# Performance work log

Hardware: AMD Instinct MI355X
Metric: run time of the kernel (lower is better)

The kernel has to match this reference:

```python
import jax, jax.numpy as jnp
import numpy as np

B, M, N_DIM = 2048, 1024, 64


def setup_inputs() -> dict:
    key = jax.random.key(0)
    ks = jax.random.split(key, 6)
    X = jax.random.normal(ks[0], (B, N_DIM), dtype=jnp.float32)
    Mu0 = jax.random.normal(ks[1], (M, N_DIM), dtype=jnp.float32)
    Mu1 = jax.random.normal(ks[2], (M, N_DIM), dtype=jnp.float32)
    # diagonal variances must be positive
    S0 = jax.random.uniform(ks[3], (M, N_DIM), dtype=jnp.float32, minval=0.1, maxval=1.0)
    S1 = jax.random.uniform(ks[4], (M, N_DIM), dtype=jnp.float32, minval=0.1, maxval=1.0)
    Lam = jax.random.uniform(ks[5], (M,), dtype=jnp.float32, minval=0.01, maxval=1.0)
    Lam = Lam / jnp.sum(Lam)  # transport-plan weights sum to 1
    return {"X": X, "Mu0": Mu0, "Mu1": Mu1, "S0": S0, "S1": S1,
            "Lam": Lam, "t": 0.3, "epsilon": 0.5}


def reference(X, Mu0, Mu1, S0, S1, Lam, t, epsilon):
    # GMMflow_fast.calc_u with sparse coupling of M nonzero (i,j) pairs.
    eps2 = epsilon ** 2
    Ds = jnp.sqrt(4.0 * S0 * S1 + epsilon ** 4)            # [M, n]
    Cs = 0.5 * (Ds - eps2)                                  # [M, n]
    v = Mu1 - Mu0                                           # [M, n]
    Mut = (1.0 - t) * Mu0 + t * Mu1                         # [M, n]
    Sigma = ((1.0 - t) ** 2) * S0 + (t ** 2) * S1 + 2.0 * t * (1.0 - t) * (Cs + 0.5 * eps2)
    Pt = t * S1 + (1.0 - t) * Cs
    Qt = (1.0 - t) * S0 + t * Cs
    St = Pt - Qt - eps2 * t
    K = St / Sigma                                          # [M, n]

    Xd = X[:, None, :] - Mut[None, :, :]                    # [B, M, n]
    U = K[None, :, :] * Xd + v[None, :, :]                  # [B, M, n]

    # Gaussian log-prob plus (n/2) log(2*pi), matching the torch code:
    # log N(x; mu, Sigma) + n/2 log(2pi) = -0.5 * sum(d^2/Sigma + log Sigma)
    logw = -0.5 * jnp.sum(Xd * Xd / Sigma[None, :, :] + jnp.log(Sigma)[None, :, :], axis=-1)  # [B, M]
    logw = jnp.clip(logw, -50.0, 50.0)
    W = jnp.exp(logw) * Lam[None, :]                        # [B, M]

    u = jnp.einsum('bm,bmd->bd', W, U)                      # [B, n]
    norm = jnp.sum(W, axis=1, keepdims=True)                # [B, 1]
    return u / norm
```

## Files before the change

### kernel.cpp

```cpp
#include <hip/hip_runtime.h>
#include <math.h>


#define B_N 2048
#define M_N 1024
#define NSPLIT 16
#define BT 64
#define MS 64

typedef short bf16x8 __attribute__((ext_vector_type(8)));
typedef float f32x4 __attribute__((ext_vector_type(4)));

static __device__ __forceinline__ unsigned short bf16rn(float f) {
    union { float f; unsigned u; } v; v.f = f;
    unsigned r = v.u + 0x7FFF + ((v.u >> 16) & 1);
    return (unsigned short)(r >> 16);
}
static __device__ __forceinline__ float bf2f(unsigned short h) {
    union { unsigned u; float f; } v; v.u = ((unsigned)h) << 16;
    return v.f;
}
static __device__ __forceinline__ void st4(unsigned short* p, unsigned short a,
                                           unsigned short b, unsigned short c, unsigned short d) {
    union { unsigned short u[4]; float2 f; } t;
    t.u[0] = a; t.u[1] = b; t.u[2] = c; t.u[3] = d;
    *(float2*)p = t.f;
}

__global__ __launch_bounds__(256)
void prep_kernel(const float* __restrict__ Mu0, const float* __restrict__ Mu1,
                 const float* __restrict__ S0, const float* __restrict__ S1,
                 const float* __restrict__ T, const float* __restrict__ E,
                 unsigned short* __restrict__ B1h, unsigned short* __restrict__ B1l,
                 unsigned short* __restrict__ VTh, float* __restrict__ qArr) {
    __shared__ float sK[4 * 65];
    __shared__ float sG[4 * 65];
    const int tid = threadIdx.x;
    const int m0 = blockIdx.x * 4;
    const int mi = tid >> 6, d = tid & 63;
    const int m = m0 + mi;
    const float t = T[0], e = E[0];
    const float eps2 = e * e, eps4 = eps2 * eps2, omt = 1.f - t;
    int idx = m * 64 + d;
    float s0 = S0[idx], s1 = S1[idx];
    float mu0 = Mu0[idx], mu1 = Mu1[idx];
    float Ds = sqrtf(4.f * s0 * s1 + eps4);
    float Cs = 0.5f * (Ds - eps2);
    float sig = omt * omt * s0 + t * t * s1 + 2.f * t * omt * (Cs + 0.5f * eps2);
    float St = (t * s1 + omt * Cs) - (omt * s0 + t * Cs) - eps2 * t;
    float a = 1.f / sig;
    float K = St * a;
    float mut = omt * mu0 + t * mu1;
    float pp = -2.f * mut * a;
    float g = (mu1 - mu0) - K * mut;
    unsigned short ah = bf16rn(a);
    B1h[m * 128 + d] = ah;
    B1l[m * 128 + d] = bf16rn(a - bf2f(ah));
    unsigned short ph = bf16rn(pp);
    B1h[m * 128 + 64 + d] = ph;
    B1l[m * 128 + 64 + d] = bf16rn(pp - bf2f(ph));
    sK[mi * 65 + d] = K;
    sG[mi * 65 + d] = g;
    float qd = mut * mut * a + __logf(sig);
    #pragma unroll
    for (int off = 32; off > 0; off >>= 1) qd += __shfl_xor(qd, off, 64);
    if (d == 0) qArr[m] = qd;
    __syncthreads();
    #pragma unroll
    for (int it = 0; it < 2; it++) {
        int i = it * 256 + tid;
        int n = i >> 2, mm = i & 3;
        float v = (n < 64) ? sK[mm * 65 + n] : sG[mm * 65 + (n - 64)];
        VTh[n * M_N + m0 + mm] = bf16rn(v);
    }
}

__global__ __launch_bounds__(256, 2)
void gmm_main_kernel(const float* __restrict__ X, const float* __restrict__ Lam,
                     const unsigned short* __restrict__ B1h, const unsigned short* __restrict__ B1l,
                     const unsigned short* __restrict__ VTh,
                     const float* __restrict__ qArr,
                     unsigned short* __restrict__ partBF, float* __restrict__ partN) {
    __shared__ __align__(16) char smem_raw[70144];
    unsigned short* sm = (unsigned short*)smem_raw;
    unsigned short* sA1h = sm;
    unsigned short* sA1l = sm + 8704;
    unsigned short* sB1h = sm + 17408;
    unsigned short* sB1l = sm + 26112;
    unsigned short* sV   = sm;
    unsigned short* sW   = sm + 17408;
    float* sQ = (float*)(smem_raw + 69632);
    float* sL = (float*)(smem_raw + 69888);

    const int tid  = threadIdx.x;
    const int Boff = blockIdx.x * BT;
    const int Moff = blockIdx.y * MS;
    const int w    = tid >> 6;
    const int lane = tid & 63;
    const int c = lane & 15, q = lane >> 4;
    const int wb = w >> 1;
    const int wm = w & 1;

    {
        const float4* X4 = (const float4*)X;
        #pragma unroll
        for (int it = 0; it < 4; it++) {
            int i = it * 256 + tid;
            int b = i >> 4, dq4 = i & 15;
            float4 xv = X4[(size_t)(Boff + b) * 16 + dq4];
            float xs[4] = {xv.x, xv.y, xv.z, xv.w};
            unsigned short yh[4], yl[4], xh[4], xl[4];
            #pragma unroll
            for (int k = 0; k < 4; k++) {
                float y = xs[k] * xs[k];
                yh[k] = bf16rn(y);  yl[k] = bf16rn(y - bf2f(yh[k]));
                xh[k] = bf16rn(xs[k]);  xl[k] = bf16rn(xs[k] - bf2f(xh[k]));
            }
            int base = b * 136 + 4 * dq4;
            st4(sA1h + base, yh[0], yh[1], yh[2], yh[3]);
            st4(sA1l + base, yl[0], yl[1], yl[2], yl[3]);
            st4(sA1h + base + 64, xh[0], xh[1], xh[2], xh[3]);
            st4(sA1l + base + 64, xl[0], xl[1], xl[2], xl[3]);
        }
        const float4* gBh = (const float4*)B1h + (size_t)Moff * 16;
        const float4* gBl = (const float4*)B1l + (size_t)Moff * 16;
        #pragma unroll
        for (int it = 0; it < 4; it++) {
            int i = it * 256 + tid;
            int row = i >> 4, cc = i & 15;
            *(float4*)(sB1h + row * 136 + cc * 8) = gBh[row * 16 + cc];
            *(float4*)(sB1l + row * 136 + cc * 8) = gBl[row * 16 + cc];
        }
        if (tid < 64) sQ[tid] = qArr[Moff + tid];
        else if (tid < 128) sL[tid - 64] = Lam[Moff + tid - 64];
    }
    __syncthreads();

    f32x4 acc1[2][2];
    #pragma unroll
    for (int i = 0; i < 2; i++)
        #pragma unroll
        for (int j = 0; j < 2; j++) acc1[i][j] = (f32x4){0.f, 0.f, 0.f, 0.f};
    #pragma unroll
    for (int ks = 0; ks < 4; ks++) {
        bf16x8 Ah[2], Al[2], Bh[2], Bl[2];
        #pragma unroll
        for (int i = 0; i < 2; i++) {
            int row = wb * 32 + i * 16 + c;
            Ah[i] = *(const bf16x8*)(sA1h + row * 136 + ks * 32 + q * 8);
            Al[i] = *(const bf16x8*)(sA1l + row * 136 + ks * 32 + q * 8);
        }
        #pragma unroll
        for (int j = 0; j < 2; j++) {
            int row = wm * 32 + j * 16 + c;
            Bh[j] = *(const bf16x8*)(sB1h + row * 136 + ks * 32 + q * 8);
            Bl[j] = *(const bf16x8*)(sB1l + row * 136 + ks * 32 + q * 8);
        }
        #pragma unroll
        for (int i = 0; i < 2; i++)
            #pragma unroll
            for (int j = 0; j < 2; j++) {
                acc1[i][j] = __builtin_amdgcn_mfma_f32_16x16x32_bf16(Ah[i], Bh[j], acc1[i][j], 0, 0, 0);
                acc1[i][j] = __builtin_amdgcn_mfma_f32_16x16x32_bf16(Ah[i], Bl[j], acc1[i][j], 0, 0, 0);
                acc1[i][j] = __builtin_amdgcn_mfma_f32_16x16x32_bf16(Al[i], Bh[j], acc1[i][j], 0, 0, 0);
            }
    }
    __syncthreads();

    {
        const float4* gV = (const float4*)VTh;
        int mo8 = Moff >> 3;
        #pragma unroll
        for (int it = 0; it < 4; it++) {
            int i = it * 256 + tid;
            int row = i >> 3, cc = i & 7;
            *(float4*)(sV + row * 72 + cc * 8) = gV[(size_t)row * 128 + mo8 + cc];
        }
        float nsum[2][4];
        #pragma unroll
        for (int i = 0; i < 2; i++)
            #pragma unroll
            for (int r = 0; r < 4; r++) nsum[i][r] = 0.f;
        #pragma unroll
        for (int i = 0; i < 2; i++)
            #pragma unroll
            for (int j = 0; j < 2; j++) {
                int m = wm * 32 + j * 16 + c;
                float qm = sQ[m], lm = sL[m];
                #pragma unroll
                for (int r = 0; r < 4; r++) {
                    int bl = wb * 32 + i * 16 + q * 4 + r;
                    float lw = -0.5f * (acc1[i][j][r] + qm);
                    lw = fminf(50.f, fmaxf(-50.f, lw));
                    float wf = __expf(lw) * lm;
                    unsigned short wh = bf16rn(wf);
                    sW[bl * 72 + m] = wh;
                    nsum[i][r] += bf2f(wh);
                }
            }
        #pragma unroll
        for (int mask = 1; mask <= 8; mask <<= 1)
            #pragma unroll
            for (int i = 0; i < 2; i++)
                #pragma unroll
                for (int r = 0; r < 4; r++)
                    nsum[i][r] += __shfl_xor(nsum[i][r], mask, 64);
        if (c == 0) {
            #pragma unroll
            for (int i = 0; i < 2; i++)
                #pragma unroll
                for (int r = 0; r < 4; r++) {
                    int b = Boff + wb * 32 + i * 16 + q * 4 + r;
                    partN[((size_t)blockIdx.y * B_N + b) * 2 + wm] = nsum[i][r];
                }
        }
    }
    __syncthreads();

    f32x4 acc2[2][4];
    #pragma unroll
    for (int i = 0; i < 2; i++)
        #pragma unroll
        for (int j = 0; j < 4; j++) acc2[i][j] = (f32x4){0.f, 0.f, 0.f, 0.f};
    #pragma unroll
    for (int ks = 0; ks < 2; ks++) {
        bf16x8 Wf[2], Vf[4];
        #pragma unroll
        for (int i = 0; i < 2; i++) {
            int row = wb * 32 + i * 16 + c;
            Wf[i] = *(const bf16x8*)(sW + row * 72 + ks * 32 + q * 8);
        }
        #pragma unroll
        for (int j = 0; j < 4; j++) {
            int row = wm * 64 + j * 16 + c;
            Vf[j] = *(const bf16x8*)(sV + row * 72 + ks * 32 + q * 8);
        }
        #pragma unroll
        for (int i = 0; i < 2; i++)
            #pragma unroll
            for (int j = 0; j < 4; j++)
                acc2[i][j] = __builtin_amdgcn_mfma_f32_16x16x32_bf16(Wf[i], Vf[j], acc2[i][j], 0, 0, 0);
    }

    #pragma unroll
    for (int i = 0; i < 2; i++)
        #pragma unroll
        for (int j = 0; j < 4; j++) {
            #pragma unroll
            for (int r = 0; r < 4; r++) {
                int b = Boff + wb * 32 + i * 16 + q * 4 + r;
                int n = wm * 64 + j * 16 + c;
                partBF[((size_t)blockIdx.y * B_N + b) * 128 + n] = bf16rn(acc2[i][j][r]);
            }
        }
}

__global__ __launch_bounds__(128)
void finalize_kernel(const float* __restrict__ X, const unsigned short* __restrict__ partBF,
                     const float* __restrict__ partN, float* __restrict__ out) {
    int gid = blockIdx.x * 128 + threadIdx.x;
    int b = gid >> 4, d0 = (gid & 15) * 4;
    float a1[4] = {0.f, 0.f, 0.f, 0.f}, a2[4] = {0.f, 0.f, 0.f, 0.f}, nn = 0.f;
    #pragma unroll
    for (int s = 0; s < NSPLIT; s++) {
        const unsigned short* row = partBF + ((size_t)s * B_N + b) * 128;
        ushort4 v1 = *(const ushort4*)(row + d0);
        ushort4 v2 = *(const ushort4*)(row + 64 + d0);
        a1[0] += bf2f(v1.x); a1[1] += bf2f(v1.y); a1[2] += bf2f(v1.z); a1[3] += bf2f(v1.w);
        a2[0] += bf2f(v2.x); a2[1] += bf2f(v2.y); a2[2] += bf2f(v2.z); a2[3] += bf2f(v2.w);
        float2 nv = *(const float2*)(partN + ((size_t)s * B_N + b) * 2);
        nn += nv.x + nv.y;
    }
    float rn = 1.f / nn;
    float4 xv = *(const float4*)(X + (size_t)b * 64 + d0);
    float4 o;
    o.x = (xv.x * a1[0] + a2[0]) * rn;
    o.y = (xv.y * a1[1] + a2[1]) * rn;
    o.z = (xv.z * a1[2] + a2[2]) * rn;
    o.w = (xv.w * a1[3] + a2[3]) * rn;
    *(float4*)(out + (size_t)b * 64 + d0) = o;
}

extern "C" void kernel_launch(void* const* d_in, const int* in_sizes, int n_in,
                              void* d_out, int out_size, void* d_ws, size_t ws_size,
                              hipStream_t stream) {
    (void)in_sizes; (void)n_in; (void)out_size; (void)ws_size;
    const float* X   = (const float*)d_in[0];
    const float* Mu0 = (const float*)d_in[1];
    const float* Mu1 = (const float*)d_in[2];
    const float* S0  = (const float*)d_in[3];
    const float* S1  = (const float*)d_in[4];
    const float* Lam = (const float*)d_in[5];
    const float* T   = (const float*)d_in[6];
    const float* E   = (const float*)d_in[7];

    char* ws = (char*)d_ws;
    unsigned short* B1h   = (unsigned short*)(ws);
    unsigned short* B1l   = (unsigned short*)(ws + 262144);
    unsigned short* VTh   = (unsigned short*)(ws + 524288);
    float*          qArr  = (float*)(ws + 786432);
    unsigned short* partBF= (unsigned short*)(ws + 790528);
    float*          partN = (float*)(ws + 790528 + 8388608);

    prep_kernel<<<256, 256, 0, stream>>>(Mu0, Mu1, S0, S1, T, E, B1h, B1l, VTh, qArr);
    dim3 grid(B_N / BT, NSPLIT);
    gmm_main_kernel<<<grid, 256, 0, stream>>>(X, Lam, B1h, B1l, VTh, qArr, partBF, partN);
    finalize_kernel<<<256, 128, 0, stream>>>(X, partBF, partN, (float*)d_out);
}
```

Baseline: 83.21 us.

## Fuse prep, main, and finalize kernels into one persistent kernel with grid barriers

Merges the three launches into a single kernel of 512 blocks, using software grid barriers (atomic counter plus spin) between the parameter-prep, GMM main, and finalize phases. Each block preps two mixture components and, after the second barrier, finalizes a 256-element slice of the output. The aim is to remove launch overhead and inter-kernel gaps. It adds a memset launch and spin-wait cost, and it depends on all 512 blocks being co-resident, otherwise it deadlocks.

After: 254.0 us. +205.2%, slower.

```diff
diff --git a/kernel.cpp b/kernel.cpp
--- a/kernel.cpp
+++ b/kernel.cpp
@@ -27,60 +27,28 @@
     *(float2*)p = t.f;
 }
 
-__global__ __launch_bounds__(256)
-void prep_kernel(const float* __restrict__ Mu0, const float* __restrict__ Mu1,
-                 const float* __restrict__ S0, const float* __restrict__ S1,
-                 const float* __restrict__ T, const float* __restrict__ E,
-                 unsigned short* __restrict__ B1h, unsigned short* __restrict__ B1l,
-                 unsigned short* __restrict__ VTh, float* __restrict__ qArr) {
-    __shared__ float sK[4 * 65];
-    __shared__ float sG[4 * 65];
-    const int tid = threadIdx.x;
-    const int m0 = blockIdx.x * 4;
-    const int mi = tid >> 6, d = tid & 63;
-    const int m = m0 + mi;
-    const float t = T[0], e = E[0];
-    const float eps2 = e * e, eps4 = eps2 * eps2, omt = 1.f - t;
-    int idx = m * 64 + d;
-    float s0 = S0[idx], s1 = S1[idx];
-    float mu0 = Mu0[idx], mu1 = Mu1[idx];
-    float Ds = sqrtf(4.f * s0 * s1 + eps4);
-    float Cs = 0.5f * (Ds - eps2);
-    float sig = omt * omt * s0 + t * t * s1 + 2.f * t * omt * (Cs + 0.5f * eps2);
-    float St = (t * s1 + omt * Cs) - (omt * s0 + t * Cs) - eps2 * t;
-    float a = 1.f / sig;
-    float K = St * a;
-    float mut = omt * mu0 + t * mu1;
-    float pp = -2.f * mut * a;
-    float g = (mu1 - mu0) - K * mut;
-    unsigned short ah = bf16rn(a);
-    B1h[m * 128 + d] = ah;
-    B1l[m * 128 + d] = bf16rn(a - bf2f(ah));
-    unsigned short ph = bf16rn(pp);
-    B1h[m * 128 + 64 + d] = ph;
-    B1l[m * 128 + 64 + d] = bf16rn(pp - bf2f(ph));
-    sK[mi * 65 + d] = K;
-    sG[mi * 65 + d] = g;
-    float qd = mut * mut * a + __logf(sig);
-    #pragma unroll
-    for (int off = 32; off > 0; off >>= 1) qd += __shfl_xor(qd, off, 64);
-    if (d == 0) qArr[m] = qd;
-    __syncthreads();
-    #pragma unroll
-    for (int it = 0; it < 2; it++) {
-        int i = it * 256 + tid;
-        int n = i >> 2, mm = i & 3;
-        float v = (n < 64) ? sK[mm * 65 + n] : sG[mm * 65 + (n - 64)];
-        VTh[n * M_N + m0 + mm] = bf16rn(v);
-    }
+static __device__ __forceinline__ void grid_barrier(int* cnt, int target, int tid) {
+    __syncthreads();
+    if (tid == 0) {
+        __threadfence();
+        atomicAdd(cnt, 1);
+        while (__hip_atomic_load(cnt, __ATOMIC_ACQUIRE, __HIP_MEMORY_SCOPE_AGENT) < target)
+            __builtin_amdgcn_s_sleep(2);
+    }
+    __syncthreads();
+    __threadfence();
 }
 
 __global__ __launch_bounds__(256, 2)
-void gmm_main_kernel(const float* __restrict__ X, const float* __restrict__ Lam,
-                     const unsigned short* __restrict__ B1h, const unsigned short* __restrict__ B1l,
-                     const unsigned short* __restrict__ VTh,
-                     const float* __restrict__ qArr,
-                     unsigned short* __restrict__ partBF, float* __restrict__ partN) {
+void gmm_fused_kernel(const float* __restrict__ X,
+                      const float* __restrict__ Mu0, const float* __restrict__ Mu1,
+                      const float* __restrict__ S0, const float* __restrict__ S1,
+                      const float* __restrict__ Lam,
+                      const float* __restrict__ T, const float* __restrict__ E,
+                      unsigned short* __restrict__ B1h, unsigned short* __restrict__ B1l,
+                      unsigned short* __restrict__ VTh, float* __restrict__ qArr,
+                      unsigned short* __restrict__ partBF, float* __restrict__ partN,
+                      int* __restrict__ cnt, float* __restrict__ out) {
     __shared__ __align__(16) char smem_raw[70144];
     unsigned short* sm = (unsigned short*)smem_raw;
     unsigned short* sA1h = sm;
@@ -93,6 +61,7 @@
     float* sL = (float*)(smem_raw + 69888);
 
     const int tid  = threadIdx.x;
+    const int bid  = blockIdx.y * 32 + blockIdx.x;
     const int Boff = blockIdx.x * BT;
     const int Moff = blockIdx.y * MS;
     const int w    = tid >> 6;
@@ -100,6 +69,39 @@
     const int c = lane & 15, q = lane >> 4;
     const int wb = w >> 1;
     const int wm = w & 1;
+
+    if (tid < 128) {
+        const int mi = tid >> 6, d = tid & 63;
+        const int m = bid * 2 + mi;
+        const float t = T[0], e = E[0];
+        const float eps2 = e * e, eps4 = eps2 * eps2, omt = 1.f - t;
+        int idx = m * 64 + d;
+        float s0 = S0[idx], s1 = S1[idx];
+        float mu0 = Mu0[idx], mu1 = Mu1[idx];
+        float Ds = sqrtf(4.f * s0 * s1 + eps4);
+        float Cs = 0.5f * (Ds - eps2);
+        float sig = omt * omt * s0 + t * t * s1 + 2.f * t * omt * (Cs + 0.5f * eps2);
+        float St = (t * s1 + omt * Cs) - (omt * s0 + t * Cs) - eps2 * t;
+        float a = 1.f / sig;
+        float K = St * a;
+        float mut = omt * mu0 + t * mu1;
+        float pp = -2.f * mut * a;
+        float g = (mu1 - mu0) - K * mut;
+        unsigned short ah = bf16rn(a);
+        B1h[m * 128 + d] = ah;
+        B1l[m * 128 + d] = bf16rn(a - bf2f(ah));
+        unsigned short ph = bf16rn(pp);
+        B1h[m * 128 + 64 + d] = ph;
+        B1l[m * 128 + 64 + d] = bf16rn(pp - bf2f(ph));
+        VTh[d * M_N + m]        = bf16rn(K);
+        VTh[(64 + d) * M_N + m] = bf16rn(g);
+        float qd = mut * mut * a + __logf(sig);
+        #pragma unroll
+        for (int off = 32; off > 0; off >>= 1) qd += __shfl_xor(qd, off, 64);
+        if (d == 0) qArr[m] = qd;
+    }
+
+    grid_barrier(cnt, 512, tid);
 
     {
         const float4* X4 = (const float4*)X;
@@ -253,32 +255,24 @@
                 partBF[((size_t)blockIdx.y * B_N + b) * 128 + n] = bf16rn(acc2[i][j][r]);
             }
         }
-}
-
-__global__ __launch_bounds__(128)
-void finalize_kernel(const float* __restrict__ X, const unsigned short* __restrict__ partBF,
-                     const float* __restrict__ partN, float* __restrict__ out) {
-    int gid = blockIdx.x * 128 + threadIdx.x;
-    int b = gid >> 4, d0 = (gid & 15) * 4;
-    float a1[4] = {0.f, 0.f, 0.f, 0.f}, a2[4] = {0.f, 0.f, 0.f, 0.f}, nn = 0.f;
-    #pragma unroll
-    for (int s = 0; s < NSPLIT; s++) {
-        const unsigned short* row = partBF + ((size_t)s * B_N + b) * 128;
-        ushort4 v1 = *(const ushort4*)(row + d0);
-        ushort4 v2 = *(const ushort4*)(row + 64 + d0);
-        a1[0] += bf2f(v1.x); a1[1] += bf2f(v1.y); a1[2] += bf2f(v1.z); a1[3] += bf2f(v1.w);
-        a2[0] += bf2f(v2.x); a2[1] += bf2f(v2.y); a2[2] += bf2f(v2.z); a2[3] += bf2f(v2.w);
-        float2 nv = *(const float2*)(partN + ((size_t)s * B_N + b) * 2);
-        nn += nv.x + nv.y;
-    }
-    float rn = 1.f / nn;
-    float4 xv = *(const float4*)(X + (size_t)b * 64 + d0);
-    float4 o;
-    o.x = (xv.x * a1[0] + a2[0]) * rn;
-    o.y = (xv.y * a1[1] + a2[1]) * rn;
-    o.z = (xv.z * a1[2] + a2[2]) * rn;
-    o.w = (xv.w * a1[3] + a2[3]) * rn;
-    *(float4*)(out + (size_t)b * 64 + d0) = o;
+
+    grid_barrier(cnt, 1024, tid);
+
+    {
+        int gid = bid * 256 + tid;
+        int b = gid >> 6, d = gid & 63;
+        float a1 = 0.f, a2 = 0.f, nn = 0.f;
+        #pragma unroll
+        for (int s = 0; s < NSPLIT; s++) {
+            const unsigned short* row = partBF + ((size_t)s * B_N + b) * 128;
+            a1 += bf2f(row[d]);
+            a2 += bf2f(row[64 + d]);
+            float2 nv = *(const float2*)(partN + ((size_t)s * B_N + b) * 2);
+            nn += nv.x + nv.y;
+        }
+        float rn = 1.f / nn;
+        out[gid] = (X[gid] * a1 + a2) * rn;
+    }
 }
 
 extern "C" void kernel_launch(void* const* d_in, const int* in_sizes, int n_in,
@@ -295,15 +289,17 @@
     const float* E   = (const float*)d_in[7];
 
     char* ws = (char*)d_ws;
-    unsigned short* B1h   = (unsigned short*)(ws);
-    unsigned short* B1l   = (unsigned short*)(ws + 262144);
-    unsigned short* VTh   = (unsigned short*)(ws + 524288);
-    float*          qArr  = (float*)(ws + 786432);
-    unsigned short* partBF= (unsigned short*)(ws + 790528);
-    float*          partN = (float*)(ws + 790528 + 8388608);
-
-    prep_kernel<<<256, 256, 0, stream>>>(Mu0, Mu1, S0, S1, T, E, B1h, B1l, VTh, qArr);
+    int*            cnt   = (int*)ws;
+    unsigned short* B1h   = (unsigned short*)(ws + 256);
+    unsigned short* B1l   = (unsigned short*)(ws + 256 + 262144);
+    unsigned short* VTh   = (unsigned short*)(ws + 256 + 524288);
+    float*          qArr  = (float*)(ws + 256 + 786432);
+    unsigned short* partBF= (unsigned short*)(ws + 256 + 790528);
+    float*          partN = (float*)(ws + 256 + 790528 + 8388608);
+
+    hipMemsetAsync(cnt, 0, 4, stream);
     dim3 grid(B_N / BT, NSPLIT);
-    gmm_main_kernel<<<grid, 256, 0, stream>>>(X, Lam, B1h, B1l, VTh, qArr, partBF, partN);
-    finalize_kernel<<<256, 128, 0, stream>>>(X, partBF, partN, (float*)d_out);
-}
+    gmm_fused_kernel<<<grid, 256, 0, stream>>>(X, Mu0, Mu1, S0, S1, Lam, T, E,
+                                               B1h, B1l, VTh, qArr, partBF, partN,
+                                               cnt, (float*)d_out);
+}
```
